# Kernel tuning notes

Measured on AMD Instinct MI355X. Metric: run time of the kernel, lower is better.

Reference implementation:

```python
import jax, jax.numpy as jnp
import numpy as np

# dims
B_, DM, DI, DS, DTR, DT_, G_, E_, K_, DC = 512, 1024, 2048, 64, 64, 64, 8, 4, 2, 4
# B_ batch, DM d_model, DI d_inner (expand*d_model), DS d_state, DTR dt_rank,
# DT_ D_time, G_ KAN grid size, E_ num_experts, K_ top_k, DC d_conv


def setup_inputs() -> dict:
    key = jax.random.key(0)
    ks = jax.random.split(key, 16)
    def n(i, shape, s=0.02):
        return jax.random.normal(ks[i], shape, dtype=jnp.float32) * s
    return {
        "uk_current_input": jax.random.normal(ks[0], (B_, DM), dtype=jnp.float32),
        "tk_current": jax.random.uniform(ks[1], (B_, 1), dtype=jnp.float32),
        "tk_previous": jax.random.uniform(ks[2], (B_, 1), dtype=jnp.float32),
        # input_proj
        "W_in": n(3, (DM, DM)), "b_in": jnp.zeros((DM,), jnp.float32),
        # K_MOTE router + sinusoidal time experts
        "router_W": n(4, (E_, 1), 1.0), "router_b": jnp.zeros((E_,), jnp.float32),
        "freq": jax.random.uniform(ks[5], (E_, DT_), minval=0.1, maxval=10.0),
        "phase": n(6, (E_, DT_), 1.0),
        "kan_W": n(7, (DT_, DT_, G_), 0.1),
        # Mamba SSM params
        "W_inproj": n(8, (2 * DI, DM)),
        "conv_w": n(9, (DI, DC), 0.1), "conv_b": jnp.zeros((DI,), jnp.float32),
        "W_x": n(10, (DTR + 2 * DS, DI)),
        "W_dt": n(11, (DI, DTR)), "dt_bias": jnp.full((DI,), -4.0, jnp.float32),
        "W_delta": n(12, (DI, DT_)),
        "A_log": jnp.log(jnp.tile(jnp.arange(1, DS + 1, dtype=jnp.float32), (DI, 1))),
        "D_skip": jnp.ones((DI,), jnp.float32),
        "W_out": n(13, (DM, DI)),
    }


def _k_mote(t, router_W, router_b, freq, phase):
    # t: (B,1) -> embedding (B, D_time), weights (B,E), mask (B,E)
    logits = t @ router_W.T + router_b                      # (B,E)
    w = jax.nn.softmax(logits, axis=-1)
    _, top_idx = jax.lax.top_k(w, K_)
    mask = jax.nn.one_hot(top_idx, E_, dtype=w.dtype).sum(axis=1)  # (B,E) binary
    w_sel = w * mask
    w_norm = w_sel / (w_sel.sum(axis=-1, keepdims=True) + 1e-8)
    # expert sinusoidal embeddings: (B,E,D_time)
    emb = jnp.sin(t[:, :, None] * freq[None] + phase[None])
    out = jnp.einsum('be,bed->bd', w_norm, emb)
    return out, w, mask


def _kan(x, kan_W):
    # rkhs_gaussian basis on fixed grid in [-1,1]
    grid = jnp.linspace(-1.0, 1.0, G_, dtype=x.dtype)
    h = 2.0 / (G_ - 1)
    phi = jnp.exp(-jnp.square((x[..., None] - grid) / h))   # (B, D_time, G)
    return jnp.einsum('big,oig->bo', phi, kan_W)


def _mamba_step(u, dt_emb, W_inproj, conv_w, conv_b, W_x, W_dt, dt_bias,
                W_delta, A_log, D_skip, W_out):
    # single-timestep selective scan (seq_len=1, zero initial state)
    xz = u @ W_inproj.T                                     # (B, 2*DI)
    x, z = jnp.split(xz, 2, axis=-1)
    # causal depthwise conv over a length-1 sequence with zero left-pad:
    # only the last kernel tap contributes
    x = x * conv_w[:, -1] + conv_b
    x = jax.nn.silu(x)
    x_dbl = x @ W_x.T                                       # (B, DTR+2*DS)
    dt_r = x_dbl[:, :DTR]
    Bmat = x_dbl[:, DTR:DTR + DS]                           # (B, DS)
    Cmat = x_dbl[:, DTR + DS:]                              # (B, DS)
    # dt modulated by the K-MOTE/KAN delta-time embedding
    dt = jax.nn.softplus(dt_r @ W_dt.T + dt_emb @ W_delta.T + dt_bias)  # (B, DI)
    # h_prev = 0 so exp(dt*A)*h_prev vanishes; h = (dt*B) * x
    h = (dt * x)[:, :, None] * Bmat[:, None, :]             # (B, DI, DS)
    y = jnp.einsum('bds,bs->bd', h, Cmat) + D_skip * x
    y = y * jax.nn.silu(z)
    return y @ W_out.T                                      # (B, DM)


def reference(uk_current_input, tk_current, tk_previous, W_in, b_in,
              router_W, router_b, freq, phase, kan_W, W_inproj, conv_w, conv_b,
              W_x, W_dt, dt_bias, W_delta, A_log, D_skip, W_out):
    processed_uk = uk_current_input @ W_in.T + b_in
    emb_tk, expert_weights, expert_mask = _k_mote(tk_current, router_W, router_b, freq, phase)
    emb_tk_prev, _, _ = _k_mote(tk_previous, router_W, router_b, freq, phase)
    delta_t_emb = _kan(emb_tk, kan_W) - _kan(emb_tk_prev, kan_W)
    hk = _mamba_step(processed_uk, delta_t_emb, W_inproj, conv_w, conv_b,
                     W_x, W_dt, dt_bias, W_delta, A_log, D_skip, W_out)
    return hk, expert_weights, expert_mask
```

## Files before the change

kernel.cpp:

```cpp
#include <hip/hip_runtime.h>
#include <hip/hip_bf16.h>
#include <math.h>

#define B_  512
#define DM  1024
#define DI  2048
#define DS  64
#define DTR 64
#define DT  64
#define G_  8
#define E_  4
#define DC  4

typedef __bf16 bf16x8 __attribute__((ext_vector_type(8)));
typedef float  f32x4  __attribute__((ext_vector_type(4)));
typedef unsigned short ushort_t;

__device__ __forceinline__ float bf2f(__hip_bfloat16 h) { return __bfloat162float(h); }
__device__ __forceinline__ __hip_bfloat16 f2bf(float f) { return __float2bfloat16(f); }
__device__ __forceinline__ float sigmoidf_(float x){ return 1.f/(1.f+expf(-x)); }
__device__ __forceinline__ float siluf_(float x){ return x*sigmoidf_(x); }
__device__ __forceinline__ float softplusf_(float x){ return (x>20.f)? x : log1pf(expf(x)); }

__device__ __forceinline__ unsigned int pack2(float a, float b) {
  unsigned short ua = __builtin_bit_cast(unsigned short, (__bf16)a);
  unsigned short ub = __builtin_bit_cast(unsigned short, (__bf16)b);
  return (unsigned int)ua | ((unsigned int)ub << 16);
}
__device__ __forceinline__ uint4 cvt8(float4 v0, float4 v1) {
  uint4 r;
  r.x = pack2(v0.x, v0.y); r.y = pack2(v0.z, v0.w);
  r.z = pack2(v1.x, v1.y); r.w = pack2(v1.z, v1.w);
  return r;
}

enum EpiKind { EPI_PART=0, EPI_G2=1, EPI_G4=2 };

struct KParams {
  const float *uk, *tk_c, *tk_p, *W_in, *b_in, *rW, *rb, *freq, *phase, *kanW;
  const float *W_inproj, *conv_w, *conv_b, *W_x, *W_dt, *dt_bias, *W_delta, *D_skip, *W_out;
  __hip_bfloat16 *Pu, *Xs, *Sz, *Yb, *Acat;
  __hip_bfloat16 *uk_bf, *Win_bf, *Wip_bf, *Wx_bf, *Wdt128, *Wout_bf;
  float *bc, *Part, *out_hk, *out_w, *out_mask;
};

__device__ __forceinline__ void cvt_chunk(const float* __restrict__ s,
                                          __hip_bfloat16* __restrict__ d)
{
  float4 v0 = *reinterpret_cast<const float4*>(s);
  float4 v1 = *reinterpret_cast<const float4*>(s + 4);
  *reinterpret_cast<uint4*>(d) = cvt8(v0, v1);
}

__global__ __launch_bounds__(256)
void convert_kernel(KParams p)
{
  const int id = blockIdx.x, t = threadIdx.x;
  if (id < 256)       { size_t c = (size_t)id*256 + t;        cvt_chunk(p.uk      + c*8, p.uk_bf  + c*8); }
  else if (id < 768)  { size_t c = (size_t)(id-256)*256 + t;  cvt_chunk(p.W_in    + c*8, p.Win_bf + c*8); }
  else if (id < 2816) { size_t c = (size_t)(id-768)*256 + t;  cvt_chunk(p.W_inproj+ c*8, p.Wip_bf + c*8); }
  else if (id < 3008) { size_t c = (size_t)(id-2816)*256 + t; cvt_chunk(p.W_x     + c*8, p.Wx_bf  + c*8); }
  else if (id < 4032) { size_t c = (size_t)(id-3008)*256 + t; cvt_chunk(p.W_out   + c*8, p.Wout_bf+ c*8); }
  else {               size_t c = (size_t)(id-4032)*256 + t;
    int row = (int)(c >> 4), col0 = ((int)c & 15)*8;
    const float* s = (col0 < 64) ? (p.W_dt    + (size_t)row*64 + col0)
                                 : (p.W_delta + (size_t)row*64 + (col0-64));
    cvt_chunk(s, p.Wdt128 + (size_t)row*128 + col0);
  }
}

template<int BM, int BN, int WMT, int WNT, int EK>
__device__ __forceinline__ void gemm_tile(char* smemc, int bxi, int byi, int bzi,
    const __hip_bfloat16* __restrict__ Ap, const __hip_bfloat16* __restrict__ Bp,
    float* __restrict__ Coutp, int Ka, int Kb, int kLen, int N, const KParams& p)
{
  static_assert(BM == 32*WMT && BN == 32*WNT, "2x2 wave layout");
  constexpr int BK = 128, SA = 136;
  constexpr int NA = (BM*BK)/(256*8);
  constexpr int NB = (BN*BK)/(256*8);
  ushort_t* sA = (ushort_t*)smemc;
  ushort_t* sB = (ushort_t*)(smemc + (size_t)2*BM*SA*sizeof(ushort_t));
  const int tid  = threadIdx.x;
  const int wave = tid >> 6, lane = tid & 63;
  const int wm = wave >> 1, wn = wave & 1;
  const int r = lane & 15, q = lane >> 4;
  const int bm = byi * BM, bn = bxi * BN;
  const int kBase = bzi * kLen;
  const int T = kLen / BK;

  uint4 ua[NA], ub[NB];

  auto loadTiles = [&](int k0) {
    #pragma unroll
    for (int c=0;c<NA;++c) {
      int idx = tid*8 + c*2048; int row = idx>>7, kk = idx&127;
      ua[c] = *reinterpret_cast<const uint4*>(Ap + (size_t)(bm+row)*Ka + k0 + kk);
    }
    #pragma unroll
    for (int c=0;c<NB;++c) {
      int idx = tid*8 + c*2048; int row = idx>>7, kk = idx&127;
      ub[c] = *reinterpret_cast<const uint4*>(Bp + (size_t)(bn+row)*Kb + k0 + kk);
    }
  };
  auto writeTiles = [&](int buf) {
    #pragma unroll
    for (int c=0;c<NA;++c) {
      int idx = tid*8 + c*2048; int row = idx>>7, kk = idx&127;
      *reinterpret_cast<uint4*>(&sA[buf*(BM*SA) + row*SA + kk]) = ua[c];
    }
    #pragma unroll
    for (int c=0;c<NB;++c) {
      int idx = tid*8 + c*2048; int row = idx>>7, kk = idx&127;
      *reinterpret_cast<uint4*>(&sB[buf*(BN*SA) + row*SA + kk]) = ub[c];
    }
  };

  f32x4 acc[WMT][WNT];
  #pragma unroll
  for (int i=0;i<WMT;++i)
    #pragma unroll
    for (int j=0;j<WNT;++j) acc[i][j] = (f32x4){0.f,0.f,0.f,0.f};

  loadTiles(kBase);
  writeTiles(0);
  for (int t=0; t<T; ++t) {
    __syncthreads();
    const int cur = t & 1;
    if (t+1 < T) loadTiles(kBase + (t+1)*BK);
    #pragma unroll
    for (int ks=0; ks<4; ++ks) {
      bf16x8 af[WMT], bfr[WNT];
      #pragma unroll
      for (int mt=0; mt<WMT; ++mt)
        af[mt] = *reinterpret_cast<const bf16x8*>(&sA[cur*(BM*SA) + (wm*(WMT*16)+mt*16+r)*SA + ks*32 + q*8]);
      #pragma unroll
      for (int nt=0; nt<WNT; ++nt)
        bfr[nt] = *reinterpret_cast<const bf16x8*>(&sB[cur*(BN*SA) + (wn*(WNT*16)+nt*16+r)*SA + ks*32 + q*8]);
      #pragma unroll
      for (int mt=0; mt<WMT; ++mt)
        #pragma unroll
        for (int nt=0; nt<WNT; ++nt)
          acc[mt][nt] = __builtin_amdgcn_mfma_f32_16x16x32_bf16(af[mt], bfr[nt], acc[mt][nt], 0,0,0);
    }
    if (t+1 < T) writeTiles(cur ^ 1);
  }

  #pragma unroll
  for (int mt=0; mt<WMT; ++mt) {
    #pragma unroll
    for (int nt=0; nt<WNT; ++nt) {
      #pragma unroll
      for (int i=0;i<4;++i) {
        int grow = bm + wm*(WMT*16) + mt*16 + q*4 + i;
        int gcol = bn + wn*(WNT*16) + nt*16 + r;
        float v = acc[mt][nt][i];
        if constexpr (EK == EPI_PART) {
          float* P = Coutp + (size_t)bzi * ((size_t)B_*N);
          P[(size_t)grow*N + gcol] = v;
        } else if constexpr (EK == EPI_G2) {
          if (gcol < DI) {
            float xc = v * p.conv_w[gcol*DC + (DC-1)] + p.conv_b[gcol];
            p.Xs[(size_t)grow*DI + gcol] = f2bf(siluf_(xc));
          } else {
            p.Sz[(size_t)grow*DI + (gcol - DI)] = f2bf(siluf_(v));
          }
        } else {
          float dt  = softplusf_(v + p.dt_bias[gcol]);
          float xsv = bf2f(p.Xs[(size_t)grow*DI + gcol]);
          float szv = bf2f(p.Sz[(size_t)grow*DI + gcol]);
          float y = (dt * xsv * p.bc[grow] + p.D_skip[gcol] * xsv) * szv;
          p.Yb[(size_t)grow*DI + gcol] = f2bf(y);
        }
      }
    }
  }
}


__device__ __forceinline__ void route(float t, const float* rW, const float* rb,
                                      float* w, float* mask, float* wn)
{
  float l[E_];
  float m = -1e30f;
  for (int e=0;e<E_;++e){ l[e] = t*rW[e] + rb[e]; m = fmaxf(m, l[e]); }
  float s = 0.f;
  for (int e=0;e<E_;++e){ w[e] = expf(l[e]-m); s += w[e]; }
  for (int e=0;e<E_;++e) w[e] /= s;
  int i1 = 0;
  for (int e=1;e<E_;++e) if (w[e] > w[i1]) i1 = e;
  int i2 = -1;
  for (int e=0;e<E_;++e) if (e != i1 && (i2 < 0 || w[e] > w[i2])) i2 = e;
  float ssel = w[i1] + w[i2] + 1e-8f;
  for (int e=0;e<E_;++e){
    float mk = (e==i1 || e==i2) ? 1.f : 0.f;
    mask[e] = mk;
    wn[e] = mk * w[e] / ssel;
  }
}

__device__ __forceinline__ void kan_job(char* smemc, int job, const KParams& p)
{
  float* dphi   = (float*)smemc;
  float* kchunk = dphi + 4*512;
  const int tid = threadIdx.x;
  const int wv = tid >> 6, lane = tid & 63;
  const int b = job*4 + wv;
  {
    float t  = p.tk_c[b];
    float tp = p.tk_p[b];
    float w_c[E_], mk_c[E_], wn_c[E_];
    float w_p[E_], mk_p[E_], wn_p[E_];
    route(t,  p.rW, p.rb, w_c, mk_c, wn_c);
    route(tp, p.rW, p.rb, w_p, mk_p, wn_p);
    if (lane < E_) {
      p.out_w[b*E_ + lane]    = w_c[lane];
      p.out_mask[b*E_ + lane] = mk_c[lane];
    }
    float ec = 0.f, epv = 0.f;
    #pragma unroll
    for (int e=0;e<E_;++e) {
      float f  = p.freq[e*DT + lane];
      float ph = p.phase[e*DT + lane];
      ec  += wn_c[e] * sinf(t*f + ph);
      epv += wn_p[e] * sinf(tp*f + ph);
    }
    const float h = 2.f/(G_-1);
    #pragma unroll
    for (int g=0; g<G_; ++g) {
      float gr = -1.f + g*h;
      float a  = (ec - gr)/h;
      float bb = (epv - gr)/h;
      dphi[wv*512 + lane*G_ + g] = expf(-a*a) - expf(-bb*bb);
    }
  }

  float accv = 0.f;
  #pragma unroll
  for (int c=0;c<4;++c) {
    __syncthreads();
    {
      const int rr = tid >> 2, seg = tid & 3;
      const float* src = p.kanW + (size_t)rr*512 + c*128 + seg*32;
      float* dst = kchunk + rr*132 + seg*32;
      #pragma unroll
      for (int i=0;i<8;++i)
        *reinterpret_cast<float4*>(dst + i*4) = *reinterpret_cast<const float4*>(src + i*4);
    }
    __syncthreads();
    const float* kr = kchunk + lane*132;
    const float* dd = dphi + wv*512 + c*128;
    #pragma unroll
    for (int j=0;j<128;j+=4) {
      float4 kv = *reinterpret_cast<const float4*>(kr + j);
      float4 dv = *reinterpret_cast<const float4*>(dd + j);
      accv += kv.x*dv.x + kv.y*dv.y + kv.z*dv.z + kv.w*dv.w;
    }
  }
  p.Acat[b*128 + 64 + lane] = f2bf(accv);
}


#define GEMM_SMEM(BM,BN) ((2*(BM)*136 + 2*(BN)*136)*2)

__global__ __launch_bounds__(256)
void g1kan_kernel(KParams p)
{
  __shared__ __align__(16) char smem[GEMM_SMEM(32,64)];
  const int id = blockIdx.x;
  if (id < 128) {
    kan_job(smem, id, p);
  } else {
    const int id2 = id - 128;
    const int bxi = id2 & 15, byi = (id2 >> 4) & 15, bzi = id2 >> 8;
    gemm_tile<32,64,1,2,EPI_PART>(smem, bxi, byi, bzi,
        p.uk_bf, p.Win_bf, p.Part, DM, DM, 256, DM, p);
  }
}

__global__ __launch_bounds__(256)
void g2_kernel(KParams p)
{
  __shared__ __align__(16) char smem[GEMM_SMEM(32,64)];
  const int bxi = blockIdx.x & 63, byi = blockIdx.x >> 6;
  gemm_tile<32,64,1,2,EPI_G2>(smem, bxi, byi, 0, p.Pu, p.Wip_bf, nullptr, DM, DM, DM, 2*DI, p);
}

__global__ __launch_bounds__(256)
void g3_kernel(KParams p)
{
  __shared__ __align__(16) char smem[GEMM_SMEM(32,64)];
  const int bxi = blockIdx.x % 3, rem = blockIdx.x / 3;
  const int byi = rem & 15, bzi = rem >> 4;
  gemm_tile<32,64,1,2,EPI_PART>(smem, bxi, byi, bzi, p.Xs, p.Wx_bf, p.Part, DI, DI, 256, 192, p);
}

__global__ __launch_bounds__(256)
void g4_kernel(KParams p)
{
  __shared__ __align__(16) char smem[GEMM_SMEM(32,64)];
  const int bxi = blockIdx.x & 31, byi = blockIdx.x >> 5;
  gemm_tile<32,64,1,2,EPI_G4>(smem, bxi, byi, 0, p.Acat, p.Wdt128, nullptr, 128, 128, 128, DI, p);
}

__global__ __launch_bounds__(256)
void g5_kernel(KParams p)
{
  __shared__ __align__(16) char smem[GEMM_SMEM(32,64)];
  const int bxi = blockIdx.x & 15, rem = blockIdx.x >> 4;
  const int byi = rem & 15, bzi = rem >> 4;
  gemm_tile<32,64,1,2,EPI_PART>(smem, bxi, byi, bzi, p.Yb, p.Wout_bf, p.Part, DI, DI, 512, DM, p);
}

__global__ __launch_bounds__(256)
void reduce_bias_kernel(KParams p)
{
  const int i = blockIdx.x*256 + threadIdx.x;
  const int total = B_*DM/4;
  const float4* pp = (const float4*)p.Part;
  float4 s = pp[i];
  #pragma unroll
  for (int k=1;k<4;++k){ float4 t = pp[i + k*total]; s.x+=t.x; s.y+=t.y; s.z+=t.z; s.w+=t.w; }
  float4 bv = ((const float4*)p.b_in)[i & (DM/4 - 1)];
  uint2 o; o.x = pack2(s.x+bv.x, s.y+bv.y); o.y = pack2(s.z+bv.z, s.w+bv.w);
  ((uint2*)p.Pu)[i] = o;
}

__global__ __launch_bounds__(192)
void reduce_g3_kernel(KParams p)
{
  const int row = blockIdx.x, col = threadIdx.x;
  const int stride = B_*192;
  float s = 0.f;
  #pragma unroll
  for (int k=0;k<8;++k) s += p.Part[(size_t)k*stride + row*192 + col];
  __shared__ float sBC[128];
  if (col < 64) p.Acat[row*128 + col] = f2bf(s);
  else          sBC[col-64] = s;
  __syncthreads();
  if (col < 64) {
    float pval = sBC[col] * sBC[col+64];
    #pragma unroll
    for (int off=32; off; off>>=1) pval += __shfl_down(pval, off);
    if (col == 0) p.bc[row] = pval;
  }
}

__global__ __launch_bounds__(256)
void reduce_plain_kernel(KParams p)
{
  const int i = blockIdx.x*256 + threadIdx.x;
  const int total = B_*DM/4;
  const float4* pp = (const float4*)p.Part;
  float4 s = pp[i];
  #pragma unroll
  for (int k=1;k<4;++k){ float4 t = pp[i + k*total]; s.x+=t.x; s.y+=t.y; s.z+=t.z; s.w+=t.w; }
  ((float4*)p.out_hk)[i] = s;
}

extern "C" void kernel_launch(void* const* d_in, const int* in_sizes, int n_in,
                              void* d_out, int out_size, void* d_ws, size_t ws_size,
                              hipStream_t stream)
{
  KParams p;
  p.uk       = (const float*)d_in[0];
  p.tk_c     = (const float*)d_in[1];
  p.tk_p     = (const float*)d_in[2];
  p.W_in     = (const float*)d_in[3];
  p.b_in     = (const float*)d_in[4];
  p.rW       = (const float*)d_in[5];
  p.rb       = (const float*)d_in[6];
  p.freq     = (const float*)d_in[7];
  p.phase    = (const float*)d_in[8];
  p.kanW     = (const float*)d_in[9];
  p.W_inproj = (const float*)d_in[10];
  p.conv_w   = (const float*)d_in[11];
  p.conv_b   = (const float*)d_in[12];
  p.W_x      = (const float*)d_in[13];
  p.W_dt     = (const float*)d_in[14];
  p.dt_bias  = (const float*)d_in[15];
  p.W_delta  = (const float*)d_in[16];
  p.D_skip   = (const float*)d_in[18];
  p.W_out    = (const float*)d_in[19];

  char* ws = (char*)d_ws;
  p.Pu     = (__hip_bfloat16*)(ws);
  p.Xs     = (__hip_bfloat16*)(ws + (size_t)(1<<20));
  p.Sz     = (__hip_bfloat16*)(ws + (size_t)3*(1<<20));
  p.Yb     = (__hip_bfloat16*)(ws + (size_t)5*(1<<20));
  p.Acat   = (__hip_bfloat16*)(ws + (size_t)7*(1<<20));
  p.bc     = (float*)         (ws + (size_t)7*(1<<20) + (128<<10));
  p.Part   = (float*)         (ws + (size_t)8*(1<<20));
  p.uk_bf  = (__hip_bfloat16*)(ws + (size_t)16*(1<<20));
  p.Win_bf = (__hip_bfloat16*)(ws + (size_t)17*(1<<20));
  p.Wip_bf = (__hip_bfloat16*)(ws + (size_t)19*(1<<20));
  p.Wx_bf  = (__hip_bfloat16*)(ws + (size_t)27*(1<<20));
  p.Wdt128 = (__hip_bfloat16*)(ws + (size_t)28*(1<<20));
  p.Wout_bf= (__hip_bfloat16*)(ws + (size_t)29*(1<<20));

  p.out_hk   = (float*)d_out;
  p.out_w    = p.out_hk + (size_t)B_*DM;
  p.out_mask = p.out_w  + (size_t)B_*E_;

  convert_kernel<<<dim3(4160), 256, 0, stream>>>(p);

  g1kan_kernel<<<dim3(1152), 256, 0, stream>>>(p);
  reduce_bias_kernel<<<dim3(512), 256, 0, stream>>>(p);

  g2_kernel<<<dim3(1024), 256, 0, stream>>>(p);

  g3_kernel<<<dim3(384), 256, 0, stream>>>(p);
  reduce_g3_kernel<<<dim3(512), 192, 0, stream>>>(p);

  g4_kernel<<<dim3(512), 256, 0, stream>>>(p);

  g5_kernel<<<dim3(1024), 256, 0, stream>>>(p);
  reduce_plain_kernel<<<dim3(512), 256, 0, stream>>>(p);
}
```

Measured before the change: 175.9 us.

## Fuse weight conversion into first GEMM launch and convert G1 operands on load

Removes the separate fp32-to-bf16 conversion kernel. The first GEMM now reads the fp32 input and W_in directly and converts them to bf16 while staging into shared memory. The remaining weight conversions run as extra blocks of the same launch as the KAN and G1 work. This saves one kernel launch and the bf16 round-trip for uk and W_in, at the cost of doubling the G1 global-load bytes and adding register pressure for the fp32 staging.

```diff
diff --git a/kernel.cpp b/kernel.cpp
--- a/kernel.cpp
+++ b/kernel.cpp
@@ -40,7 +40,7 @@
   const float *uk, *tk_c, *tk_p, *W_in, *b_in, *rW, *rb, *freq, *phase, *kanW;
   const float *W_inproj, *conv_w, *conv_b, *W_x, *W_dt, *dt_bias, *W_delta, *D_skip, *W_out;
   __hip_bfloat16 *Pu, *Xs, *Sz, *Yb, *Acat;
-  __hip_bfloat16 *uk_bf, *Win_bf, *Wip_bf, *Wx_bf, *Wdt128, *Wout_bf;
+  __hip_bfloat16 *Wip_bf, *Wx_bf, *Wdt128, *Wout_bf;
   float *bc, *Part, *out_hk, *out_w, *out_mask;
 };
 
@@ -52,26 +52,9 @@
   *reinterpret_cast<uint4*>(d) = cvt8(v0, v1);
 }
 
-__global__ __launch_bounds__(256)
-void convert_kernel(KParams p)
-{
-  const int id = blockIdx.x, t = threadIdx.x;
-  if (id < 256)       { size_t c = (size_t)id*256 + t;        cvt_chunk(p.uk      + c*8, p.uk_bf  + c*8); }
-  else if (id < 768)  { size_t c = (size_t)(id-256)*256 + t;  cvt_chunk(p.W_in    + c*8, p.Win_bf + c*8); }
-  else if (id < 2816) { size_t c = (size_t)(id-768)*256 + t;  cvt_chunk(p.W_inproj+ c*8, p.Wip_bf + c*8); }
-  else if (id < 3008) { size_t c = (size_t)(id-2816)*256 + t; cvt_chunk(p.W_x     + c*8, p.Wx_bf  + c*8); }
-  else if (id < 4032) { size_t c = (size_t)(id-3008)*256 + t; cvt_chunk(p.W_out   + c*8, p.Wout_bf+ c*8); }
-  else {               size_t c = (size_t)(id-4032)*256 + t;
-    int row = (int)(c >> 4), col0 = ((int)c & 15)*8;
-    const float* s = (col0 < 64) ? (p.W_dt    + (size_t)row*64 + col0)
-                                 : (p.W_delta + (size_t)row*64 + (col0-64));
-    cvt_chunk(s, p.Wdt128 + (size_t)row*128 + col0);
-  }
-}
-
-template<int BM, int BN, int WMT, int WNT, int EK>
+template<int BM, int BN, int WMT, int WNT, int EK, bool CVTA, bool CVTB>
 __device__ __forceinline__ void gemm_tile(char* smemc, int bxi, int byi, int bzi,
-    const __hip_bfloat16* __restrict__ Ap, const __hip_bfloat16* __restrict__ Bp,
+    const void* __restrict__ Ap, const void* __restrict__ Bp,
     float* __restrict__ Coutp, int Ka, int Kb, int kLen, int N, const KParams& p)
 {
   static_assert(BM == 32*WMT && BN == 32*WNT, "2x2 wave layout");
@@ -89,29 +72,44 @@
   const int T = kLen / BK;
 
   uint4 ua[NA], ub[NB];
+  float4 fa[NA][2], fb[NB][2];
 
   auto loadTiles = [&](int k0) {
     #pragma unroll
     for (int c=0;c<NA;++c) {
       int idx = tid*8 + c*2048; int row = idx>>7, kk = idx&127;
-      ua[c] = *reinterpret_cast<const uint4*>(Ap + (size_t)(bm+row)*Ka + k0 + kk);
+      if constexpr (CVTA) {
+        const float* s = (const float*)Ap + (size_t)(bm+row)*Ka + k0 + kk;
+        fa[c][0] = *reinterpret_cast<const float4*>(s);
+        fa[c][1] = *reinterpret_cast<const float4*>(s+4);
+      } else {
+        ua[c] = *reinterpret_cast<const uint4*>((const __hip_bfloat16*)Ap + (size_t)(bm+row)*Ka + k0 + kk);
+      }
     }
     #pragma unroll
     for (int c=0;c<NB;++c) {
       int idx = tid*8 + c*2048; int row = idx>>7, kk = idx&127;
-      ub[c] = *reinterpret_cast<const uint4*>(Bp + (size_t)(bn+row)*Kb + k0 + kk);
+      if constexpr (CVTB) {
+        const float* s = (const float*)Bp + (size_t)(bn+row)*Kb + k0 + kk;
+        fb[c][0] = *reinterpret_cast<const float4*>(s);
+        fb[c][1] = *reinterpret_cast<const float4*>(s+4);
+      } else {
+        ub[c] = *reinterpret_cast<const uint4*>((const __hip_bfloat16*)Bp + (size_t)(bn+row)*Kb + k0 + kk);
+      }
     }
   };
   auto writeTiles = [&](int buf) {
     #pragma unroll
     for (int c=0;c<NA;++c) {
       int idx = tid*8 + c*2048; int row = idx>>7, kk = idx&127;
-      *reinterpret_cast<uint4*>(&sA[buf*(BM*SA) + row*SA + kk]) = ua[c];
+      uint4 v; if constexpr (CVTA) v = cvt8(fa[c][0], fa[c][1]); else v = ua[c];
+      *reinterpret_cast<uint4*>(&sA[buf*(BM*SA) + row*SA + kk]) = v;
     }
     #pragma unroll
     for (int c=0;c<NB;++c) {
       int idx = tid*8 + c*2048; int row = idx>>7, kk = idx&127;
-      *reinterpret_cast<uint4*>(&sB[buf*(BN*SA) + row*SA + kk]) = ub[c];
+      uint4 v; if constexpr (CVTB) v = cvt8(fb[c][0], fb[c][1]); else v = ub[c];
+      *reinterpret_cast<uint4*>(&sB[buf*(BN*SA) + row*SA + kk]) = v;
     }
   };
 
@@ -263,17 +261,25 @@
 #define GEMM_SMEM(BM,BN) ((2*(BM)*136 + 2*(BN)*136)*2)
 
 __global__ __launch_bounds__(256)
-void g1kan_kernel(KParams p)
+void g1kan_conv_kernel(KParams p)
 {
   __shared__ __align__(16) char smem[GEMM_SMEM(32,64)];
-  const int id = blockIdx.x;
+  const int id = blockIdx.x, t = threadIdx.x;
   if (id < 128) {
     kan_job(smem, id, p);
-  } else {
+  } else if (id < 1152) {
     const int id2 = id - 128;
     const int bxi = id2 & 15, byi = (id2 >> 4) & 15, bzi = id2 >> 8;
-    gemm_tile<32,64,1,2,EPI_PART>(smem, bxi, byi, bzi,
-        p.uk_bf, p.Win_bf, p.Part, DM, DM, 256, DM, p);
+    gemm_tile<32,64,1,2,EPI_PART,true,true>(smem, bxi, byi, bzi,
+        p.uk, p.W_in, p.Part, DM, DM, 256, DM, p);
+  } else if (id < 3200) { size_t c = (size_t)(id-1152)*256 + t; cvt_chunk(p.W_inproj + c*8, p.Wip_bf  + c*8); }
+  else if (id < 3392)   { size_t c = (size_t)(id-3200)*256 + t; cvt_chunk(p.W_x      + c*8, p.Wx_bf   + c*8); }
+  else if (id < 4416)   { size_t c = (size_t)(id-3392)*256 + t; cvt_chunk(p.W_out    + c*8, p.Wout_bf + c*8); }
+  else {                  size_t c = (size_t)(id-4416)*256 + t;
+    int row = (int)(c >> 4), col0 = ((int)c & 15)*8;
+    const float* s = (col0 < 64) ? (p.W_dt    + (size_t)row*64 + col0)
+                                 : (p.W_delta + (size_t)row*64 + (col0-64));
+    cvt_chunk(s, p.Wdt128 + (size_t)row*128 + col0);
   }
 }
 
@@ -282,7 +288,7 @@
 {
   __shared__ __align__(16) char smem[GEMM_SMEM(32,64)];
   const int bxi = blockIdx.x & 63, byi = blockIdx.x >> 6;
-  gemm_tile<32,64,1,2,EPI_G2>(smem, bxi, byi, 0, p.Pu, p.Wip_bf, nullptr, DM, DM, DM, 2*DI, p);
+  gemm_tile<32,64,1,2,EPI_G2,false,false>(smem, bxi, byi, 0, p.Pu, p.Wip_bf, nullptr, DM, DM, DM, 2*DI, p);
 }
 
 __global__ __launch_bounds__(256)
@@ -291,7 +297,7 @@
   __shared__ __align__(16) char smem[GEMM_SMEM(32,64)];
   const int bxi = blockIdx.x % 3, rem = blockIdx.x / 3;
   const int byi = rem & 15, bzi = rem >> 4;
-  gemm_tile<32,64,1,2,EPI_PART>(smem, bxi, byi, bzi, p.Xs, p.Wx_bf, p.Part, DI, DI, 256, 192, p);
+  gemm_tile<32,64,1,2,EPI_PART,false,false>(smem, bxi, byi, bzi, p.Xs, p.Wx_bf, p.Part, DI, DI, 256, 192, p);
 }
 
 __global__ __launch_bounds__(256)
@@ -299,7 +305,7 @@
 {
   __shared__ __align__(16) char smem[GEMM_SMEM(32,64)];
   const int bxi = blockIdx.x & 31, byi = blockIdx.x >> 5;
-  gemm_tile<32,64,1,2,EPI_G4>(smem, bxi, byi, 0, p.Acat, p.Wdt128, nullptr, 128, 128, 128, DI, p);
+  gemm_tile<32,64,1,2,EPI_G4,false,false>(smem, bxi, byi, 0, p.Acat, p.Wdt128, nullptr, 128, 128, 128, DI, p);
 }
 
 __global__ __launch_bounds__(256)
@@ -308,7 +314,7 @@
   __shared__ __align__(16) char smem[GEMM_SMEM(32,64)];
   const int bxi = blockIdx.x & 15, rem = blockIdx.x >> 4;
   const int byi = rem & 15, bzi = rem >> 4;
-  gemm_tile<32,64,1,2,EPI_PART>(smem, bxi, byi, bzi, p.Yb, p.Wout_bf, p.Part, DI, DI, 512, DM, p);
+  gemm_tile<32,64,1,2,EPI_PART,false,false>(smem, bxi, byi, bzi, p.Yb, p.Wout_bf, p.Part, DI, DI, 512, DM, p);
 }
 
 __global__ __launch_bounds__(256)
@@ -390,8 +396,6 @@
   p.Acat   = (__hip_bfloat16*)(ws + (size_t)7*(1<<20));
   p.bc     = (float*)         (ws + (size_t)7*(1<<20) + (128<<10));
   p.Part   = (float*)         (ws + (size_t)8*(1<<20));
-  p.uk_bf  = (__hip_bfloat16*)(ws + (size_t)16*(1<<20));
-  p.Win_bf = (__hip_bfloat16*)(ws + (size_t)17*(1<<20));
   p.Wip_bf = (__hip_bfloat16*)(ws + (size_t)19*(1<<20));
   p.Wx_bf  = (__hip_bfloat16*)(ws + (size_t)27*(1<<20));
   p.Wdt128 = (__hip_bfloat16*)(ws + (size_t)28*(1<<20));
@@ -401,9 +405,7 @@
   p.out_w    = p.out_hk + (size_t)B_*DM;
   p.out_mask = p.out_w  + (size_t)B_*E_;
 
-  convert_kernel<<<dim3(4160), 256, 0, stream>>>(p);
-
-  g1kan_kernel<<<dim3(1152), 256, 0, stream>>>(p);
+  g1kan_conv_kernel<<<dim3(4544), 256, 0, stream>>>(p);
   reduce_bias_kernel<<<dim3(512), 256, 0, stream>>>(p);
 
   g2_kernel<<<dim3(1024), 256, 0, stream>>>(p);
```

Result: faster. 169.1 us (-3.9%).
